# Performance work log

Measured on AMD Instinct MI355X. Metric: run time of the kernel, lower is better.

## Reference

```python
import jax, jax.numpy as jnp
import numpy as np

N_NODES = 50000
N_EDGES = 800000
D = 128        # node_attr_dim
E_DIM = 32     # edge radial basis dim
LN_EPS = 1e-5


def setup_inputs() -> dict:
    key = jax.random.key(0)
    ks = jax.random.split(key, 8)
    return {
        "node_attr": jax.random.normal(ks[0], (N_NODES, D), dtype=jnp.float32),
        "edge_attr": jax.random.normal(ks[1], (N_EDGES, E_DIM), dtype=jnp.float32),
        "edge_index": jax.random.randint(ks[2], (2, N_EDGES), 0, N_NODES, dtype=jnp.int64),
        "W_node": jax.random.normal(ks[3], (D, D), dtype=jnp.float32),
        "W_center_node": jax.random.normal(ks[4], (D, D), dtype=jnp.float32),
        "W_concat_node": jax.random.normal(ks[5], (2 * D, D), dtype=jnp.float32),
        "W_edge": jax.random.normal(ks[6], (E_DIM, D), dtype=jnp.float32),
        "ln_weight": jnp.ones((D,), dtype=jnp.float32),
        "ln_bias": jnp.zeros((D,), dtype=jnp.float32),
    }


def _layernorm(x, w, b):
    mu = jnp.mean(x, axis=-1, keepdims=True)
    var = jnp.mean(jnp.square(x - mu), axis=-1, keepdims=True)
    return (x - mu) * jax.lax.rsqrt(var + LN_EPS) * w + b


def reference(node_attr, edge_attr, edge_index, W_node, W_center_node,
              W_concat_node, W_edge, ln_weight, ln_bias):
    edge_center = edge_index[0]
    edge_neigh = edge_index[1]
    num_nodes = node_attr.shape[0]

    proj_node = node_attr @ W_node                       # [N, D]
    proj_edge = proj_node[edge_neigh]                    # [E, D] gather
    proj_radial = edge_attr @ W_edge                     # [E, D]
    m_node = jax.ops.segment_sum(proj_edge * proj_radial, edge_center,
                                 num_segments=num_nodes)  # [N, D] scatter_sum

    proj_center_node = node_attr @ W_center_node         # [N, D]
    cat = jnp.concatenate([proj_center_node, m_node], axis=-1)  # [N, 2D]
    h_node = _layernorm(cat @ W_concat_node, ln_weight, ln_bias)  # [N, D]
    return h_node
```

## Files before the change

### kernel.cpp

```cpp
#include <hip/hip_runtime.h>

#define ND 128
#define ED 32
#define LN_EPS 1e-5f

typedef __attribute__((ext_vector_type(8))) short bf16x8;
typedef __attribute__((ext_vector_type(4))) float f32x4;

__device__ __forceinline__ unsigned short f32_to_bf16(float f) {
    const unsigned u = __float_as_uint(f);
    return (unsigned short)((u + 0x7FFFu + ((u >> 16) & 1u)) >> 16);
}
__device__ __forceinline__ float bf16f(unsigned short h) {
    return __uint_as_float(((unsigned)h) << 16);
}

__global__ void conv_hist_kernel(const unsigned* __restrict__ raw,
                                 int* __restrict__ cnt, int E) {
    __shared__ int s_is64;
    if (threadIdx.x == 0) {
        unsigned acc = 0;
        for (int i = 1; i < 512; i += 2) acc |= raw[i];
        s_is64 = (acc == 0) ? 1 : 0;
    }
    __syncthreads();
    const int is64 = s_is64;
    const int tid = blockIdx.x * blockDim.x + threadIdx.x;
    const int stride = gridDim.x * blockDim.x;
    if (is64) {
        for (int e = tid; e < E; e += stride)
            atomicAdd(&cnt[(int)raw[(size_t)2 * e]], 1);
    } else {
        for (int e = tid; e < E; e += stride)
            atomicAdd(&cnt[(int)raw[e]], 1);
    }
}

__global__ __launch_bounds__(256) void scan1_kernel(
    const int* __restrict__ cnt, int* __restrict__ sum1,
    int* __restrict__ sum2, int N) {
    __shared__ int l1[256], l2[256];
    const int t = threadIdx.x;
    const int i = blockIdx.x * 256 + t;
    const int c = (i < N) ? cnt[i] : 0;
    l1[t] = c;
    l2[t] = (c + 15) & ~15;
    __syncthreads();
    for (int off = 128; off > 0; off >>= 1) {
        if (t < off) { l1[t] += l1[t + off]; l2[t] += l2[t + off]; }
        __syncthreads();
    }
    if (t == 0) { sum1[blockIdx.x] = l1[0]; sum2[blockIdx.x] = l2[0]; }
}

__global__ __launch_bounds__(1024) void scan2_kernel(
    int* __restrict__ sum1, int* __restrict__ sum2,
    int* __restrict__ base, int* __restrict__ pbase, int NB, int N) {
    __shared__ int l1[1024], l2[1024];
    const int t = threadIdx.x;
    const int v1 = (t < NB) ? sum1[t] : 0;
    const int v2 = (t < NB) ? sum2[t] : 0;
    l1[t] = v1; l2[t] = v2;
    __syncthreads();
    for (int off = 1; off < 1024; off <<= 1) {
        int a = 0, b = 0;
        if (t >= off) { a = l1[t - off]; b = l2[t - off]; }
        __syncthreads();
        l1[t] += a; l2[t] += b;
        __syncthreads();
    }
    if (t < NB) {
        sum1[t] = l1[t] - v1;
        sum2[t] = l2[t] - v2;
    }
    if (t == NB - 1) { base[N] = l1[t]; pbase[N] = l2[t]; }
}

__global__ __launch_bounds__(256) void scan3_kernel(
    const int* __restrict__ cnt, const int* __restrict__ sum1,
    const int* __restrict__ sum2, int* __restrict__ base,
    int* __restrict__ pbase, int* __restrict__ cur, int N) {
    __shared__ int l1[256], l2[256];
    const int t = threadIdx.x;
    const int i = blockIdx.x * 256 + t;
    const int c = (i < N) ? cnt[i] : 0;
    const int p = (c + 15) & ~15;
    l1[t] = c; l2[t] = p;
    __syncthreads();
    for (int off = 1; off < 256; off <<= 1) {
        int a = 0, b = 0;
        if (t >= off) { a = l1[t - off]; b = l2[t - off]; }
        __syncthreads();
        l1[t] += a; l2[t] += b;
        __syncthreads();
    }
    if (i < N) {
        base[i]  = sum1[blockIdx.x] + l1[t] - c;
        pbase[i] = sum2[blockIdx.x] + l2[t] - p;
        cur[i] = 0;
    }
}

__global__ __launch_bounds__(256) void padfill_kernel(
    const int* __restrict__ cnt, const int* __restrict__ pbase,
    int2* __restrict__ epad, int N) {
    const int v = blockIdx.x * 256 + threadIdx.x;
    if (v < N) {
        const int s = pbase[v] + cnt[v];
        const int t = pbase[v + 1];
        for (int p = s; p < t; ++p) epad[p] = make_int2(0, 0);
    }
    if (blockIdx.x == 0 && threadIdx.x < 64) {
        const int tail = pbase[N];
        epad[tail + threadIdx.x] = make_int2(0, 0);
    }
}

__global__ void scatter_kernel(const unsigned* __restrict__ raw,
                               const int* __restrict__ pbase,
                               int* __restrict__ cur,
                               int2* __restrict__ epad, int E) {
    __shared__ int s_is64;
    if (threadIdx.x == 0) {
        unsigned acc = 0;
        for (int i = 1; i < 512; i += 2) acc |= raw[i];
        s_is64 = (acc == 0) ? 1 : 0;
    }
    __syncthreads();
    const int is64 = s_is64;
    const int tid = blockIdx.x * blockDim.x + threadIdx.x;
    const int stride = gridDim.x * blockDim.x;
    if (is64) {
        for (int e = tid; e < E; e += stride) {
            const int c = (int)raw[(size_t)2 * e];
            const int n = (int)raw[(size_t)2 * E + (size_t)2 * e];
            const int pos = pbase[c] + atomicAdd(&cur[c], 1);
            epad[pos] = make_int2(e, n);
        }
    } else {
        for (int e = tid; e < E; e += stride) {
            const int c = (int)raw[e];
            const int n = (int)raw[(size_t)E + e];
            const int pos = pbase[c] + atomicAdd(&cur[c], 1);
            epad[pos] = make_int2(e, n);
        }
    }
}

__global__ void wcc_kernel(const float* __restrict__ Wc,
                           const float* __restrict__ Wcat,
                           float* __restrict__ wcc) {
    const int i = blockIdx.x;
    const int j = threadIdx.x;
    float acc = 0.f;
    for (int k = 0; k < ND; ++k)
        acc += Wc[i * ND + k] * Wcat[k * ND + j];
    wcc[i * ND + j] = acc;
}

__global__ __launch_bounds__(512, 4) void gemm128_kernel(
    const float* __restrict__ A, const float* __restrict__ W,
    float* __restrict__ out, int M) {
    __shared__ float Ws[ND * ND];
    {
        float4* d = (float4*)Ws;
        const float4* s = (const float4*)W;
        for (int i = threadIdx.x; i < (ND * ND) / 4; i += 512) d[i] = s[i];
    }
    __syncthreads();
    const int slot = (int)(threadIdx.x >> 5);
    const int j0 = ((int)threadIdx.x & 31) * 4;
    const int rbase = blockIdx.x * 64 + slot * 4;
    const int r0 = (rbase + 0 < M) ? rbase + 0 : M - 1;
    const int r1 = (rbase + 1 < M) ? rbase + 1 : M - 1;
    const int r2 = (rbase + 2 < M) ? rbase + 2 : M - 1;
    const int r3 = (rbase + 3 < M) ? rbase + 3 : M - 1;
    const float* ap0 = A + (size_t)r0 * ND;
    const float* ap1 = A + (size_t)r1 * ND;
    const float* ap2 = A + (size_t)r2 * ND;
    const float* ap3 = A + (size_t)r3 * ND;
    float4 acc0 = {0,0,0,0}, acc1 = {0,0,0,0};
    float4 acc2 = {0,0,0,0}, acc3 = {0,0,0,0};
#pragma unroll 2
    for (int c = 0; c < 32; ++c) {
        const float4 a0 = *(const float4*)(ap0 + c * 4);
        const float4 a1 = *(const float4*)(ap1 + c * 4);
        const float4 a2 = *(const float4*)(ap2 + c * 4);
        const float4 a3 = *(const float4*)(ap3 + c * 4);
#pragma unroll
        for (int kk = 0; kk < 4; ++kk) {
            const float4 w = *(const float4*)&Ws[(c * 4 + kk) * ND + j0];
            const float x0 = ((const float*)&a0)[kk];
            const float x1 = ((const float*)&a1)[kk];
            const float x2 = ((const float*)&a2)[kk];
            const float x3 = ((const float*)&a3)[kk];
            acc0.x += x0 * w.x; acc0.y += x0 * w.y;
            acc0.z += x0 * w.z; acc0.w += x0 * w.w;
            acc1.x += x1 * w.x; acc1.y += x1 * w.y;
            acc1.z += x1 * w.z; acc1.w += x1 * w.w;
            acc2.x += x2 * w.x; acc2.y += x2 * w.y;
            acc2.z += x2 * w.z; acc2.w += x2 * w.w;
            acc3.x += x3 * w.x; acc3.y += x3 * w.y;
            acc3.z += x3 * w.z; acc3.w += x3 * w.w;
        }
    }
    if (rbase + 0 < M) *(float4*)&out[(size_t)r0 * ND + j0] = acc0;
    if (rbase + 1 < M) *(float4*)&out[(size_t)r1 * ND + j0] = acc1;
    if (rbase + 2 < M) *(float4*)&out[(size_t)r2 * ND + j0] = acc2;
    if (rbase + 3 < M) *(float4*)&out[(size_t)r3 * ND + j0] = acc3;
}

__global__ __launch_bounds__(256) void seg_mfma_kernel(
    const int* __restrict__ base, const int* __restrict__ pbase,
    const int2* __restrict__ epad, const float* __restrict__ edge_attr,
    const float* __restrict__ W_edge, const float* __restrict__ P,
    float* __restrict__ m, int N, int CPW) {
    const int l   = (int)threadIdx.x & 63;
    const int r16 = l & 15;
    const int kg  = l >> 4;
    bf16x8 bh[8], bl[8];
#pragma unroll
    for (int t = 0; t < 8; ++t) {
#pragma unroll
        for (int j = 0; j < 8; ++j) {
            const float wv = W_edge[(kg * 8 + j) * ND + t * 16 + r16];
            const unsigned short h = f32_to_bf16(wv);
            bh[t][j] = (short)h;
            bl[t][j] = (short)f32_to_bf16(wv - bf16f(h));
        }
    }
    const f32x4 zero = {0.f, 0.f, 0.f, 0.f};
    const int wid = blockIdx.x * 4 + ((int)threadIdx.x >> 6);
    const int v0 = wid * CPW;
    if (v0 >= N) return;
    const int v1 = min(v0 + CPW, N);

    int pos = pbase[v0];
    int2 epA = epad[pos + r16];
    int2 epB = epad[pos + 16 + r16];
    float4 xA, yA, xB, yB;
    {
        const float* ap = edge_attr + (size_t)epA.x * ED + kg * 8;
        xA = *(const float4*)ap; yA = *(const float4*)(ap + 4);
        const float* bp = edge_attr + (size_t)epB.x * ED + kg * 8;
        xB = *(const float4*)bp; yB = *(const float4*)(bp + 4);
    }

    for (int v = v0; v < v1; ++v) {
        const int vend = pbase[v] + (base[v + 1] - base[v]);
        const int pend = pbase[v + 1];
        float part[8] = {0.f, 0.f, 0.f, 0.f, 0.f, 0.f, 0.f, 0.f};
        while (pos < pend) {
            const int2 epC = epad[pos + 32 + r16];
            float4 x = xA, y = yA;
            if (pos + r16 >= vend) {
                x.x = x.y = x.z = x.w = 0.f;
                y = x;
            }
            bf16x8 ah, al;
#pragma unroll
            for (int j = 0; j < 4; ++j) {
                const float fx = ((const float*)&x)[j];
                const unsigned short hx = f32_to_bf16(fx);
                ah[j] = (short)hx;
                al[j] = (short)f32_to_bf16(fx - bf16f(hx));
                const float fy = ((const float*)&y)[j];
                const unsigned short hy = f32_to_bf16(fy);
                ah[4 + j] = (short)hy;
                al[4 + j] = (short)f32_to_bf16(fy - bf16f(hy));
            }
            const int n0 = __shfl(epA.y, kg * 4 + 0, 16);
            const int n1 = __shfl(epA.y, kg * 4 + 1, 16);
            const int n2 = __shfl(epA.y, kg * 4 + 2, 16);
            const int n3 = __shfl(epA.y, kg * 4 + 3, 16);
            const float* q0 = P + (size_t)n0 * ND + r16;
            const float* q1 = P + (size_t)n1 * ND + r16;
            const float* q2 = P + (size_t)n2 * ND + r16;
            const float* q3 = P + (size_t)n3 * ND + r16;
#pragma unroll
            for (int t = 0; t < 8; ++t) {
                f32x4 D = __builtin_amdgcn_mfma_f32_16x16x32_bf16(
                    ah, bh[t], zero, 0, 0, 0);
                D = __builtin_amdgcn_mfma_f32_16x16x32_bf16(
                    al, bh[t], D, 0, 0, 0);
                D = __builtin_amdgcn_mfma_f32_16x16x32_bf16(
                    ah, bl[t], D, 0, 0, 0);
                part[t] += D[0] * q0[t * 16];
                part[t] += D[1] * q1[t * 16];
                part[t] += D[2] * q2[t * 16];
                part[t] += D[3] * q3[t * 16];
            }
            epA = epB; xA = xB; yA = yB;
            epB = epC;
            const float* np = edge_attr + (size_t)epB.x * ED + kg * 8;
            xB = *(const float4*)np;
            yB = *(const float4*)(np + 4);
            pos += 16;
        }
#pragma unroll
        for (int t = 0; t < 8; ++t) {
            part[t] += __shfl_xor(part[t], 16);
            part[t] += __shfl_xor(part[t], 32);
        }
        if (l < 16) {
#pragma unroll
            for (int t = 0; t < 8; ++t)
                m[(size_t)v * ND + t * 16 + l] = part[t];
        }
    }
}

__global__ __launch_bounds__(512, 4) void final_kernel(
    const float* __restrict__ A1, const float* __restrict__ A2,
    const float* __restrict__ W1, const float* __restrict__ W2,
    const float* __restrict__ lnw, const float* __restrict__ lnb,
    float* __restrict__ out, int N) {
    __shared__ float Ws[ND * ND];
    const int slot = (int)(threadIdx.x >> 5);
    const int j0 = ((int)threadIdx.x & 31) * 4;
    const int rbase = blockIdx.x * 64 + slot * 4;
    const int r0 = (rbase + 0 < N) ? rbase + 0 : N - 1;
    const int r1 = (rbase + 1 < N) ? rbase + 1 : N - 1;
    const int r2 = (rbase + 2 < N) ? rbase + 2 : N - 1;
    const int r3 = (rbase + 3 < N) ? rbase + 3 : N - 1;
    float4 acc0 = {0,0,0,0}, acc1 = {0,0,0,0};
    float4 acc2 = {0,0,0,0}, acc3 = {0,0,0,0};

#define K_PHASE(AP, WP)                                                       \
    {                                                                         \
        {                                                                     \
            float4* d = (float4*)Ws;                                          \
            const float4* sw = (const float4*)(WP);                           \
            for (int i = threadIdx.x; i < (ND * ND) / 4; i += 512)            \
                d[i] = sw[i];                                                 \
        }                                                                     \
        __syncthreads();                                                      \
        const float* ap0 = (AP) + (size_t)r0 * ND;                            \
        const float* ap1 = (AP) + (size_t)r1 * ND;                            \
        const float* ap2 = (AP) + (size_t)r2 * ND;                            \
        const float* ap3 = (AP) + (size_t)r3 * ND;                            \
        _Pragma("unroll 2")                                                   \
        for (int c = 0; c < 32; ++c) {                                        \
            const float4 a0 = *(const float4*)(ap0 + c * 4);                  \
            const float4 a1 = *(const float4*)(ap1 + c * 4);                  \
            const float4 a2 = *(const float4*)(ap2 + c * 4);                  \
            const float4 a3 = *(const float4*)(ap3 + c * 4);                  \
            _Pragma("unroll")                                                 \
            for (int kk = 0; kk < 4; ++kk) {                                  \
                const float4 w = *(const float4*)&Ws[(c * 4 + kk) * ND + j0]; \
                const float x0 = ((const float*)&a0)[kk];                     \
                const float x1 = ((const float*)&a1)[kk];                     \
                const float x2 = ((const float*)&a2)[kk];                     \
                const float x3 = ((const float*)&a3)[kk];                     \
                acc0.x += x0 * w.x; acc0.y += x0 * w.y;                       \
                acc0.z += x0 * w.z; acc0.w += x0 * w.w;                       \
                acc1.x += x1 * w.x; acc1.y += x1 * w.y;                       \
                acc1.z += x1 * w.z; acc1.w += x1 * w.w;                       \
                acc2.x += x2 * w.x; acc2.y += x2 * w.y;                       \
                acc2.z += x2 * w.z; acc2.w += x2 * w.w;                       \
                acc3.x += x3 * w.x; acc3.y += x3 * w.y;                       \
                acc3.z += x3 * w.z; acc3.w += x3 * w.w;                       \
            }                                                                 \
        }                                                                     \
        __syncthreads();                                                      \
    }

    K_PHASE(A1, W1)
    K_PHASE(A2, W2)
#undef K_PHASE

    const float4 w4 = *(const float4*)&lnw[j0];
    const float4 b4 = *(const float4*)&lnb[j0];
#define LN_ROW(ACC, RQ, VALID)                                               \
    {                                                                        \
        float4 h = ACC;                                                      \
        float sum = h.x + h.y + h.z + h.w;                                   \
        sum += __shfl_xor(sum, 16); sum += __shfl_xor(sum, 8);               \
        sum += __shfl_xor(sum, 4);  sum += __shfl_xor(sum, 2);               \
        sum += __shfl_xor(sum, 1);                                           \
        const float mean = sum * (1.f / ND);                                 \
        const float4 dd = {h.x - mean, h.y - mean, h.z - mean, h.w - mean};  \
        float qv = dd.x * dd.x + dd.y * dd.y + dd.z * dd.z + dd.w * dd.w;    \
        qv += __shfl_xor(qv, 16); qv += __shfl_xor(qv, 8);                   \
        qv += __shfl_xor(qv, 4);  qv += __shfl_xor(qv, 2);                   \
        qv += __shfl_xor(qv, 1);                                             \
        const float rstd = rsqrtf(qv * (1.f / ND) + LN_EPS);                 \
        if (VALID) {                                                         \
            float4 o;                                                        \
            o.x = dd.x * rstd * w4.x + b4.x;                                 \
            o.y = dd.y * rstd * w4.y + b4.y;                                 \
            o.z = dd.z * rstd * w4.z + b4.z;                                 \
            o.w = dd.w * rstd * w4.w + b4.w;                                 \
            *(float4*)&out[(size_t)(RQ) * ND + j0] = o;                      \
        }                                                                    \
    }
    LN_ROW(acc0, r0, rbase + 0 < N)
    LN_ROW(acc1, r1, rbase + 1 < N)
    LN_ROW(acc2, r2, rbase + 2 < N)
    LN_ROW(acc3, r3, rbase + 3 < N)
#undef LN_ROW
}

extern "C" void kernel_launch(void* const* d_in, const int* in_sizes, int n_in,
                              void* d_out, int out_size, void* d_ws, size_t ws_size,
                              hipStream_t stream) {
    const float*    node_attr = (const float*)d_in[0];
    const float*    edge_attr = (const float*)d_in[1];
    const unsigned* edge_idx  = (const unsigned*)d_in[2];
    const float*    W_node    = (const float*)d_in[3];
    const float*    W_center  = (const float*)d_in[4];
    const float*    W_concat  = (const float*)d_in[5];
    const float*    W_edge    = (const float*)d_in[6];
    const float*    lnw       = (const float*)d_in[7];
    const float*    lnb       = (const float*)d_in[8];
    float* out = (float*)d_out;

    const int N = in_sizes[0] / ND;
    const int E = in_sizes[1] / ED;
    const int NB = (N + 255) / 256;
    const size_t PADCAP = (size_t)E + 15 * (size_t)N + 64;

    char* ws = (char*)d_ws;
    float* wcc   = (float*)ws;
    float* P     = (float*)(ws + 65536);
    float* m     = P + (size_t)N * ND;
    int2*  epad  = (int2*)(m + (size_t)N * ND);
    int*   cnt   = (int*)(epad + PADCAP);
    int*   base  = cnt + N;
    int*   pbase = base + N + 1;
    int*   cur   = pbase + N + 1;
    int*   sum1  = cur + N;
    int*   sum2  = sum1 + NB;

    hipMemsetAsync(cnt, 0, (size_t)N * sizeof(int), stream);
    conv_hist_kernel<<<512, 256, 0, stream>>>(edge_idx, cnt, E);
    scan1_kernel<<<NB, 256, 0, stream>>>(cnt, sum1, sum2, N);
    scan2_kernel<<<1, 1024, 0, stream>>>(sum1, sum2, base, pbase, NB, N);
    scan3_kernel<<<NB, 256, 0, stream>>>(cnt, sum1, sum2, base, pbase, cur, N);
    padfill_kernel<<<NB, 256, 0, stream>>>(cnt, pbase, epad, N);
    scatter_kernel<<<512, 256, 0, stream>>>(edge_idx, pbase, cur, epad, E);
    wcc_kernel<<<128, 128, 0, stream>>>(W_center, W_concat, wcc);
    gemm128_kernel<<<(N + 63) / 64, 512, 0, stream>>>(node_attr, W_node, P, N);
    {
        const int nwaves = 1024 * 4;
        const int cpw = (N + nwaves - 1) / nwaves;
        seg_mfma_kernel<<<1024, 256, 0, stream>>>(base, pbase, epad,
                                                  edge_attr, W_edge, P, m,
                                                  N, cpw);
    }
    final_kernel<<<(N + 63) / 64, 512, 0, stream>>>(node_attr, m, wcc,
                                                    W_concat + ND * ND,
                                                    lnw, lnb, out, N);
}
```

Before: 306.2 us.

## Merge padfill, scatter, node GEMM and weight-fold kernels into one launch

After: 293.8 us (median of 2 runs). -4.1%, faster.

```diff
diff --git a/kernel.cpp b/kernel.cpp
--- a/kernel.cpp
+++ b/kernel.cpp
@@ -101,113 +101,117 @@
     }
 }
 
-__global__ __launch_bounds__(256) void padfill_kernel(
-    const int* __restrict__ cnt, const int* __restrict__ pbase,
-    int2* __restrict__ epad, int N) {
-    const int v = blockIdx.x * 256 + threadIdx.x;
-    if (v < N) {
-        const int s = pbase[v] + cnt[v];
-        const int t = pbase[v + 1];
-        for (int p = s; p < t; ++p) epad[p] = make_int2(0, 0);
-    }
-    if (blockIdx.x == 0 && threadIdx.x < 64) {
-        const int tail = pbase[N];
-        epad[tail + threadIdx.x] = make_int2(0, 0);
-    }
-}
-
-__global__ void scatter_kernel(const unsigned* __restrict__ raw,
-                               const int* __restrict__ pbase,
-                               int* __restrict__ cur,
-                               int2* __restrict__ epad, int E) {
-    __shared__ int s_is64;
-    if (threadIdx.x == 0) {
-        unsigned acc = 0;
-        for (int i = 1; i < 512; i += 2) acc |= raw[i];
-        s_is64 = (acc == 0) ? 1 : 0;
-    }
-    __syncthreads();
-    const int is64 = s_is64;
-    const int tid = blockIdx.x * blockDim.x + threadIdx.x;
-    const int stride = gridDim.x * blockDim.x;
-    if (is64) {
-        for (int e = tid; e < E; e += stride) {
-            const int c = (int)raw[(size_t)2 * e];
-            const int n = (int)raw[(size_t)2 * E + (size_t)2 * e];
-            const int pos = pbase[c] + atomicAdd(&cur[c], 1);
-            epad[pos] = make_int2(e, n);
-        }
-    } else {
-        for (int e = tid; e < E; e += stride) {
-            const int c = (int)raw[e];
-            const int n = (int)raw[(size_t)E + e];
-            const int pos = pbase[c] + atomicAdd(&cur[c], 1);
-            epad[pos] = make_int2(e, n);
-        }
-    }
-}
-
-__global__ void wcc_kernel(const float* __restrict__ Wc,
-                           const float* __restrict__ Wcat,
-                           float* __restrict__ wcc) {
-    const int i = blockIdx.x;
-    const int j = threadIdx.x;
-    float acc = 0.f;
-    for (int k = 0; k < ND; ++k)
-        acc += Wc[i * ND + k] * Wcat[k * ND + j];
-    wcc[i * ND + j] = acc;
-}
-
-__global__ __launch_bounds__(512, 4) void gemm128_kernel(
+__global__ __launch_bounds__(512, 4) void fused_mid_kernel(
+    const unsigned* __restrict__ raw, const int* __restrict__ cnt,
+    const int* __restrict__ pbase, int* __restrict__ cur,
+    int2* __restrict__ epad,
     const float* __restrict__ A, const float* __restrict__ W,
-    float* __restrict__ out, int M) {
-    __shared__ float Ws[ND * ND];
+    float* __restrict__ P,
+    const float* __restrict__ Wc, const float* __restrict__ Wcat,
+    float* __restrict__ wcc,
+    int N, int E, int NPF, int NSC, int NG) {
+    const int bid = blockIdx.x;
+    if (bid < NPF) {
+        const int v = bid * 512 + (int)threadIdx.x;
+        if (v < N) {
+            const int s = pbase[v] + cnt[v];
+            const int t = pbase[v + 1];
+            for (int p = s; p < t; ++p) epad[p] = make_int2(0, 0);
+        }
+        if (bid == 0 && threadIdx.x < 64) {
+            const int tail = pbase[N];
+            epad[tail + threadIdx.x] = make_int2(0, 0);
+        }
+        return;
+    }
+    if (bid < NPF + NSC) {
+        __shared__ int s_is64;
+        if (threadIdx.x == 0) {
+            unsigned acc = 0;
+            for (int i = 1; i < 512; i += 2) acc |= raw[i];
+            s_is64 = (acc == 0) ? 1 : 0;
+        }
+        __syncthreads();
+        const int is64 = s_is64;
+        const int tid = (bid - NPF) * 512 + (int)threadIdx.x;
+        const int stride = NSC * 512;
+        if (is64) {
+            for (int e = tid; e < E; e += stride) {
+                const int c = (int)raw[(size_t)2 * e];
+                const int n = (int)raw[(size_t)2 * E + (size_t)2 * e];
+                const int pos = pbase[c] + atomicAdd(&cur[c], 1);
+                epad[pos] = make_int2(e, n);
+            }
+        } else {
+            for (int e = tid; e < E; e += stride) {
+                const int c = (int)raw[e];
+                const int n = (int)raw[(size_t)E + e];
+                const int pos = pbase[c] + atomicAdd(&cur[c], 1);
+                epad[pos] = make_int2(e, n);
+            }
+        }
+        return;
+    }
+    if (bid < NPF + NSC + NG) {
+        __shared__ float Ws[ND * ND];
+        {
+            float4* d = (float4*)Ws;
+            const float4* s = (const float4*)W;
+            for (int i = threadIdx.x; i < (ND * ND) / 4; i += 512) d[i] = s[i];
+        }
+        __syncthreads();
+        const int bg = bid - NPF - NSC;
+        const int slot = (int)(threadIdx.x >> 5);
+        const int j0 = ((int)threadIdx.x & 31) * 4;
+        const int rbase = bg * 64 + slot * 4;
+        const int r0 = (rbase + 0 < N) ? rbase + 0 : N - 1;
+        const int r1 = (rbase + 1 < N) ? rbase + 1 : N - 1;
+        const int r2 = (rbase + 2 < N) ? rbase + 2 : N - 1;
+        const int r3 = (rbase + 3 < N) ? rbase + 3 : N - 1;
+        const float* ap0 = A + (size_t)r0 * ND;
+        const float* ap1 = A + (size_t)r1 * ND;
+        const float* ap2 = A + (size_t)r2 * ND;
+        const float* ap3 = A + (size_t)r3 * ND;
+        float4 acc0 = {0,0,0,0}, acc1 = {0,0,0,0};
+        float4 acc2 = {0,0,0,0}, acc3 = {0,0,0,0};
+#pragma unroll 2
+        for (int c = 0; c < 32; ++c) {
+            const float4 a0 = *(const float4*)(ap0 + c * 4);
+            const float4 a1 = *(const float4*)(ap1 + c * 4);
+            const float4 a2 = *(const float4*)(ap2 + c * 4);
+            const float4 a3 = *(const float4*)(ap3 + c * 4);
+#pragma unroll
+            for (int kk = 0; kk < 4; ++kk) {
+                const float4 w = *(const float4*)&Ws[(c * 4 + kk) * ND + j0];
+                const float x0 = ((const float*)&a0)[kk];
+                const float x1 = ((const float*)&a1)[kk];
+                const float x2 = ((const float*)&a2)[kk];
+                const float x3 = ((const float*)&a3)[kk];
+                acc0.x += x0 * w.x; acc0.y += x0 * w.y;
+                acc0.z += x0 * w.z; acc0.w += x0 * w.w;
+                acc1.x += x1 * w.x; acc1.y += x1 * w.y;
+                acc1.z += x1 * w.z; acc1.w += x1 * w.w;
+                acc2.x += x2 * w.x; acc2.y += x2 * w.y;
+                acc2.z += x2 * w.z; acc2.w += x2 * w.w;
+                acc3.x += x3 * w.x; acc3.y += x3 * w.y;
+                acc3.z += x3 * w.z; acc3.w += x3 * w.w;
+            }
+        }
+        if (rbase + 0 < N) *(float4*)&P[(size_t)r0 * ND + j0] = acc0;
+        if (rbase + 1 < N) *(float4*)&P[(size_t)r1 * ND + j0] = acc1;
+        if (rbase + 2 < N) *(float4*)&P[(size_t)r2 * ND + j0] = acc2;
+        if (rbase + 3 < N) *(float4*)&P[(size_t)r3 * ND + j0] = acc3;
+        return;
+    }
     {
-        float4* d = (float4*)Ws;
-        const float4* s = (const float4*)W;
-        for (int i = threadIdx.x; i < (ND * ND) / 4; i += 512) d[i] = s[i];
-    }
-    __syncthreads();
-    const int slot = (int)(threadIdx.x >> 5);
-    const int j0 = ((int)threadIdx.x & 31) * 4;
-    const int rbase = blockIdx.x * 64 + slot * 4;
-    const int r0 = (rbase + 0 < M) ? rbase + 0 : M - 1;
-    const int r1 = (rbase + 1 < M) ? rbase + 1 : M - 1;
-    const int r2 = (rbase + 2 < M) ? rbase + 2 : M - 1;
-    const int r3 = (rbase + 3 < M) ? rbase + 3 : M - 1;
-    const float* ap0 = A + (size_t)r0 * ND;
-    const float* ap1 = A + (size_t)r1 * ND;
-    const float* ap2 = A + (size_t)r2 * ND;
-    const float* ap3 = A + (size_t)r3 * ND;
-    float4 acc0 = {0,0,0,0}, acc1 = {0,0,0,0};
-    float4 acc2 = {0,0,0,0}, acc3 = {0,0,0,0};
-#pragma unroll 2
-    for (int c = 0; c < 32; ++c) {
-        const float4 a0 = *(const float4*)(ap0 + c * 4);
-        const float4 a1 = *(const float4*)(ap1 + c * 4);
-        const float4 a2 = *(const float4*)(ap2 + c * 4);
-        const float4 a3 = *(const float4*)(ap3 + c * 4);
-#pragma unroll
-        for (int kk = 0; kk < 4; ++kk) {
-            const float4 w = *(const float4*)&Ws[(c * 4 + kk) * ND + j0];
-            const float x0 = ((const float*)&a0)[kk];
-            const float x1 = ((const float*)&a1)[kk];
-            const float x2 = ((const float*)&a2)[kk];
-            const float x3 = ((const float*)&a3)[kk];
-            acc0.x += x0 * w.x; acc0.y += x0 * w.y;
-            acc0.z += x0 * w.z; acc0.w += x0 * w.w;
-            acc1.x += x1 * w.x; acc1.y += x1 * w.y;
-            acc1.z += x1 * w.z; acc1.w += x1 * w.w;
-            acc2.x += x2 * w.x; acc2.y += x2 * w.y;
-            acc2.z += x2 * w.z; acc2.w += x2 * w.w;
-            acc3.x += x3 * w.x; acc3.y += x3 * w.y;
-            acc3.z += x3 * w.z; acc3.w += x3 * w.w;
-        }
-    }
-    if (rbase + 0 < M) *(float4*)&out[(size_t)r0 * ND + j0] = acc0;
-    if (rbase + 1 < M) *(float4*)&out[(size_t)r1 * ND + j0] = acc1;
-    if (rbase + 2 < M) *(float4*)&out[(size_t)r2 * ND + j0] = acc2;
-    if (rbase + 3 < M) *(float4*)&out[(size_t)r3 * ND + j0] = acc3;
+        const int bw = bid - NPF - NSC - NG;
+        const int i = bw * 4 + ((int)threadIdx.x >> 7);
+        const int j = (int)threadIdx.x & 127;
+        float acc = 0.f;
+        for (int k = 0; k < ND; ++k)
+            acc += Wc[i * ND + k] * Wcat[k * ND + j];
+        wcc[i * ND + j] = acc;
+    }
 }
 
 __global__ __launch_bounds__(256) void seg_mfma_kernel(
@@ -437,10 +441,17 @@
     scan1_kernel<<<NB, 256, 0, stream>>>(cnt, sum1, sum2, N);
     scan2_kernel<<<1, 1024, 0, stream>>>(sum1, sum2, base, pbase, NB, N);
     scan3_kernel<<<NB, 256, 0, stream>>>(cnt, sum1, sum2, base, pbase, cur, N);
-    padfill_kernel<<<NB, 256, 0, stream>>>(cnt, pbase, epad, N);
-    scatter_kernel<<<512, 256, 0, stream>>>(edge_idx, pbase, cur, epad, E);
-    wcc_kernel<<<128, 128, 0, stream>>>(W_center, W_concat, wcc);
-    gemm128_kernel<<<(N + 63) / 64, 512, 0, stream>>>(node_attr, W_node, P, N);
+    {
+        const int NPF = (N + 511) / 512;
+        const int NSC = 256;
+        const int NG  = (N + 63) / 64;
+        const int NW  = 32;
+        fused_mid_kernel<<<NPF + NSC + NG + NW, 512, 0, stream>>>(
+            edge_idx, cnt, pbase, cur, epad,
+            node_attr, W_node, P,
+            W_center, W_concat, wcc,
+            N, E, NPF, NSC, NG);
+    }
     {
         const int nwaves = 1024 * 4;
         const int cpw = (N + nwaves - 1) / nwaves;
```
